# Kernel optimization log

Hardware: AMD Instinct MI355X
Metric: run time of the kernel (lower is better)

The kernel has to match this reference:

```python
import jax, jax.numpy as jnp
import numpy as np

L = 3  # len(context)

def _scale_zp_int8(vmin, vmax):
    # calcScaleZeroPointInt8: qmin=-127, qmax=127
    scale = (vmax - vmin) / 254.0
    initial_zp = -127.0 - vmin / scale
    # clamp to [-127,127] then int() (trunc toward zero)
    zp = jnp.trunc(jnp.clip(initial_zp, -127.0, 127.0)).astype(jnp.int32)
    return scale, zp


def setup_inputs() -> dict:
    key = jax.random.key(0)
    k1, k2, k3 = jax.random.split(key, 3)
    mb, N, D, O = 1, 16386, 1024, 2048
    x = jax.random.normal(k1, (mb, N, D), dtype=jnp.float32)
    W = jax.random.normal(k2, (O, D * L), dtype=jnp.float32) * 0.05
    b = jax.random.normal(k3, (O, 1), dtype=jnp.float32) * 0.1
    return {
        "input": x,
        "weight": W,
        "bias": b,
        "input_min": jnp.min(x),
        "input_max": jnp.max(x),
    }


def reference(input, weight, bias, input_min, input_max):
    mb, N, D = input.shape
    T = N - L + 1  # expected_N
    # im2col-style context gather: window of L consecutive frames -> [mb, T, D*L]
    padded = jnp.concatenate([input[:, i:i + T, :] for i in range(L)], axis=2)

    # weight quantization (int8, symmetric range [-127,127])
    w_scale, w_zp = _scale_zp_int8(jnp.min(weight), jnp.max(weight))
    qw = jnp.round(weight / w_scale + w_zp).astype(jnp.int8)            # [O, K]
    dequant_weight = (qw.astype(jnp.float32) - w_zp.astype(jnp.float32)) * w_scale

    # input quantization
    in_scale, in_zp = _scale_zp_int8(input_min, input_max)
    qx = jnp.round(padded / in_scale + in_zp).astype(jnp.int8)          # [mb, T, K]

    qx32 = qx.astype(jnp.int32)
    qw32 = qw.astype(jnp.int32)

    # int32 GEMM + zero-point correction terms
    x1 = jnp.einsum('btk,ok->bto', qx32, qw32)      # [mb, T, O] int32
    x2 = in_zp * jnp.sum(qw32, axis=1)              # [O]
    x3 = w_zp * jnp.sum(qx32, axis=2)               # [mb, T]

    K = weight.shape[1]
    x = (x1 - x2)[0].T - x3.reshape(-1)             # [O, T]
    x = x + K * w_zp * in_zp
    x = x.T[None].astype(jnp.float32) * (in_scale * w_scale)  # [1, T, O]
    x = x + bias.T                                  # bias [O,1] -> broadcast [1,O]
    return (x, dequant_weight, bias)
```

## Files before the change

kernel.cpp:

```cpp
#include <hip/hip_runtime.h>
#include <stdint.h>

typedef __attribute__((ext_vector_type(4))) int i32x4;

#define N_FRAMES 16386
#define D_DIM    1024
#define O_DIM    2048
#define L_CTX    3
#define K_DIM    3072
#define T_DIM    16384
#define NKT      24

#define WS_PART   0u
#define WS_PARAMS 8192u
#define WS_CO     16384u
#define WS_S      32768u
#define WS_QW     262144u
#define WS_QX     8388608u

struct Params {
  float w_scale, in_scale, cscale;
  int   w_zp, in_zp, konst;
};

typedef __attribute__((address_space(3))) void       lds_void;
typedef const __attribute__((address_space(1))) void gbl_void;

__device__ __forceinline__ unsigned flip_f(float f) {
  unsigned u = __float_as_uint(f);
  return (u & 0x80000000u) ? ~u : (u | 0x80000000u);
}
__device__ __forceinline__ float unflip_f(unsigned v) {
  unsigned u = (v & 0x80000000u) ? (v ^ 0x80000000u) : ~v;
  return __uint_as_float(u);
}

__global__ __launch_bounds__(256) void wminmax_kernel(const float4* __restrict__ w,
                                                      uint2* __restrict__ part, int n4) {
  unsigned lmin = 0xFFFFFFFFu, lmax = 0u;
  for (int i = blockIdx.x * blockDim.x + threadIdx.x; i < n4; i += gridDim.x * blockDim.x) {
    float4 v = w[i];
    unsigned a = flip_f(v.x), b = flip_f(v.y), c = flip_f(v.z), d = flip_f(v.w);
    lmin = min(lmin, min(min(a, b), min(c, d)));
    lmax = max(lmax, max(max(a, b), max(c, d)));
  }
#pragma unroll
  for (int off = 32; off > 0; off >>= 1) {
    lmin = min(lmin, (unsigned)__shfl_xor((int)lmin, off, 64));
    lmax = max(lmax, (unsigned)__shfl_xor((int)lmax, off, 64));
  }
  __shared__ unsigned rmn[4], rmx[4];
  const int wv = threadIdx.x >> 6;
  if ((threadIdx.x & 63) == 0) { rmn[wv] = lmin; rmx[wv] = lmax; }
  __syncthreads();
  if (threadIdx.x == 0) {
    unsigned mn = min(min(rmn[0], rmn[1]), min(rmn[2], rmn[3]));
    unsigned mx = max(max(rmx[0], rmx[1]), max(rmx[2], rmx[3]));
    part[blockIdx.x] = make_uint2(mn, mx);
  }
}

__global__ __launch_bounds__(256) void params_kernel(const uint2* __restrict__ part,
                                                     const float* __restrict__ in_min,
                                                     const float* __restrict__ in_max,
                                                     Params* __restrict__ p) {
  const int t = threadIdx.x;
  uint2 a = part[t], b = part[t + 256];
  unsigned mn = min(a.x, b.x), mx = max(a.y, b.y);
#pragma unroll
  for (int off = 32; off > 0; off >>= 1) {
    mn = min(mn, (unsigned)__shfl_xor((int)mn, off, 64));
    mx = max(mx, (unsigned)__shfl_xor((int)mx, off, 64));
  }
  __shared__ unsigned rmn[4], rmx[4];
  const int wv = t >> 6;
  if ((t & 63) == 0) { rmn[wv] = mn; rmx[wv] = mx; }
  __syncthreads();
  if (t == 0) {
    float wmin = unflip_f(min(min(rmn[0], rmn[1]), min(rmn[2], rmn[3])));
    float wmax = unflip_f(max(max(rmx[0], rmx[1]), max(rmx[2], rmx[3])));
    float ws = (wmax - wmin) / 254.0f;
    float wz = -127.0f - wmin / ws;
    wz = fminf(fmaxf(wz, -127.0f), 127.0f);
    int wzp = (int)wz;
    float imin = *in_min, imax = *in_max;
    float is = (imax - imin) / 254.0f;
    float iz = -127.0f - imin / is;
    iz = fminf(fmaxf(iz, -127.0f), 127.0f);
    int izp = (int)iz;
    p->w_scale = ws; p->in_scale = is; p->cscale = is * ws;
    p->w_zp = wzp;   p->in_zp = izp;
    p->konst = K_DIM * wzp * izp;
  }
}

__global__ __launch_bounds__(256) void quantw_kernel(
    const float* __restrict__ w, const float* __restrict__ bias,
    const Params* __restrict__ p, int8_t* __restrict__ qw,
    int* __restrict__ co, float* __restrict__ dq, float* __restrict__ bias_out) {
  const int o = blockIdx.x;
  const float ws = p->w_scale;
  const float zpf = (float)p->w_zp;
  const float* wrow = w + (size_t)o * K_DIM;
  float* dqrow = dq + (size_t)o * K_DIM;
  int8_t* qrow = qw + (size_t)o * K_DIM;
  int sum = 0;
#pragma unroll
  for (int pass = 0; pass < 3; ++pass) {
    const int k = (pass << 10) + (threadIdx.x << 2);
    float4 v = *(const float4*)(wrow + k);
    int8_t c0 = (int8_t)(int)rintf(v.x / ws + zpf);
    int8_t c1 = (int8_t)(int)rintf(v.y / ws + zpf);
    int8_t c2 = (int8_t)(int)rintf(v.z / ws + zpf);
    int8_t c3 = (int8_t)(int)rintf(v.w / ws + zpf);
    sum += (int)c0 + (int)c1 + (int)c2 + (int)c3;
    unsigned packed = (unsigned)(uint8_t)c0 | ((unsigned)(uint8_t)c1 << 8)
                    | ((unsigned)(uint8_t)c2 << 16) | ((unsigned)(uint8_t)c3 << 24);
    *(unsigned*)(qrow + k) = packed;
    float4 d;
    d.x = ((float)c0 - zpf) * ws;
    d.y = ((float)c1 - zpf) * ws;
    d.z = ((float)c2 - zpf) * ws;
    d.w = ((float)c3 - zpf) * ws;
    *(float4*)(dqrow + k) = d;
  }
  __shared__ int red[4];
#pragma unroll
  for (int off = 32; off > 0; off >>= 1) sum += __shfl_xor(sum, off, 64);
  if ((threadIdx.x & 63) == 0) red[threadIdx.x >> 6] = sum;
  __syncthreads();
  if (threadIdx.x == 0) {
    int tot = red[0] + red[1] + red[2] + red[3];
    co[o] = -p->in_zp * tot;
    bias_out[o] = bias[o];
  }
}

__global__ __launch_bounds__(256) void quantx_kernel(
    const float* __restrict__ x, const Params* __restrict__ p,
    int8_t* __restrict__ qx, int* __restrict__ s) {
  const int n = blockIdx.x;
  const float is = p->in_scale;
  const float zpf = (float)p->in_zp;
  const float4 v = *((const float4*)(x + (size_t)n * D_DIM) + threadIdx.x);
  int8_t c0 = (int8_t)(int)rintf(v.x / is + zpf);
  int8_t c1 = (int8_t)(int)rintf(v.y / is + zpf);
  int8_t c2 = (int8_t)(int)rintf(v.z / is + zpf);
  int8_t c3 = (int8_t)(int)rintf(v.w / is + zpf);
  unsigned packed = (unsigned)(uint8_t)c0 | ((unsigned)(uint8_t)c1 << 8)
                  | ((unsigned)(uint8_t)c2 << 16) | ((unsigned)(uint8_t)c3 << 24);
  ((unsigned*)(qx + (size_t)n * D_DIM))[threadIdx.x] = packed;
  int sum = (int)c0 + (int)c1 + (int)c2 + (int)c3;
  __shared__ int red[4];
#pragma unroll
  for (int off = 32; off > 0; off >>= 1) sum += __shfl_xor(sum, off, 64);
  if ((threadIdx.x & 63) == 0) red[threadIdx.x >> 6] = sum;
  __syncthreads();
  if (threadIdx.x == 0) s[n] = red[0] + red[1] + red[2] + red[3];
}

__global__ __launch_bounds__(512, 2) void gemm_kernel(
    const int8_t* __restrict__ qx, const int8_t* __restrict__ qw,
    const int* __restrict__ co, const int* __restrict__ s,
    const float* __restrict__ bias, const Params* __restrict__ p,
    float* __restrict__ out) {
  __shared__ int8_t A_lds[2][256 * 128];
  __shared__ int8_t B_lds[2][256 * 128];

  const int bid = blockIdx.x;
  const int tn = bid & 7;
  const int tm = bid >> 3;
  const int m0 = tm << 8, n0 = tn << 8;
  const int tid = threadIdx.x;
  const int lane = tid & 63, wave = tid >> 6;
  const int wm = wave >> 2, wn = wave & 3;
  const int lr = lane & 15, kg = lane >> 4;
  const int lr7 = lane & 7;

  const int st_row = tid >> 3;
  const int st_sc  = ((tid & 7) ^ (st_row & 7)) << 4;
  const int8_t* qxa = qx + (size_t)(m0 + st_row) * D_DIM + st_sc;
  const int8_t* qwb = qw + (size_t)(n0 + st_row) * K_DIM + st_sc;

  const int c0 = (kg ^ lr7) << 4;
  const int arow = ((wm << 7) + lr) << 7;
  const int brow = ((wn << 6) + lr) << 7;

  i32x4 a[8][2], b[4][2];
  i32x4 acc[8][4] = {};

  auto stageA = [&](int buf, int kt) {
    const int8_t* sp = qxa + (kt << 7);
#pragma unroll
    for (int j = 0; j < 4; ++j)
      __builtin_amdgcn_global_load_lds((gbl_void*)(sp + (size_t)(j << 6) * D_DIM),
          (lds_void*)(&A_lds[buf][(j << 13) + (wave << 10)]), 16, 0, 0);
  };
  auto stageB = [&](int buf, int kt) {
    const int8_t* sp = qwb + (kt << 7);
#pragma unroll
    for (int j = 0; j < 4; ++j)
      __builtin_amdgcn_global_load_lds((gbl_void*)(sp + (size_t)(j << 6) * K_DIM),
          (lds_void*)(&B_lds[buf][(j << 13) + (wave << 10)]), 16, 0, 0);
  };
  auto read_full = [&](int bf) {
#pragma unroll
    for (int ks = 0; ks < 2; ++ks) {
#pragma unroll
      for (int m = 0; m < 8; ++m)
        a[m][ks] = *(const i32x4*)&A_lds[bf][arow + (m << 11) + (c0 ^ (ks << 6))];
#pragma unroll
      for (int n = 0; n < 4; ++n)
        b[n][ks] = *(const i32x4*)&B_lds[bf][brow + (n << 11) + (c0 ^ (ks << 6))];
    }
  };

  stageA(0, 0); stageB(0, 0);
  stageA(1, 1); stageB(1, 1);
  asm volatile("s_waitcnt vmcnt(8)" ::: "memory");
  __builtin_amdgcn_s_barrier();
  read_full(0);

  for (int kt = 0; kt < NKT; ++kt) {
    const int buf = kt & 1, nxt = buf ^ 1;

    asm volatile("s_waitcnt lgkmcnt(0)" ::: "memory");
    __builtin_amdgcn_s_setprio(1);
#pragma unroll
    for (int m = 0; m < 8; ++m)
#pragma unroll
      for (int n = 0; n < 4; ++n)
#pragma unroll
        for (int ks = 0; ks < 2; ++ks)
          acc[m][n] = __builtin_amdgcn_mfma_i32_16x16x64_i8(a[m][ks], b[n][ks], acc[m][n], 0, 0, 0);
    __builtin_amdgcn_s_setprio(0);

    if (kt + 1 < NKT) {
      asm volatile("s_waitcnt vmcnt(0)" ::: "memory");
      __builtin_amdgcn_s_barrier();
      read_full(nxt);
      if (kt + 2 < NKT) { stageA(buf, kt + 2); stageB(buf, kt + 2); }
    }
  }

  const float cscale = p->cscale;
  const int   wzp    = p->w_zp;
  const int   konst  = p->konst;
  int   cov[4];
  float bov[4];
#pragma unroll
  for (int n = 0; n < 4; ++n) {
    const int o_ = n0 + (wn << 6) + (n << 4) + lr;
    cov[n] = co[o_];
    bov[n] = bias[o_];
  }
#pragma unroll
  for (int m = 0; m < 8; ++m) {
    const int tbase = m0 + (wm << 7) + (m << 4) + (kg << 2);
    int sv[6];
#pragma unroll
    for (int r = 0; r < 6; ++r) sv[r] = s[tbase + r];
    int ctv[4];
#pragma unroll
    for (int r = 0; r < 4; ++r) ctv[r] = konst - wzp * (sv[r] + sv[r + 1] + sv[r + 2]);
#pragma unroll
    for (int n = 0; n < 4; ++n) {
      const int o_ = n0 + (wn << 6) + (n << 4) + lr;
#pragma unroll
      for (int r = 0; r < 4; ++r) {
        out[(size_t)(tbase + r) * O_DIM + o_] =
            (float)(acc[m][n][r] + cov[n] + ctv[r]) * cscale + bov[n];
      }
    }
  }
}

extern "C" void kernel_launch(void* const* d_in, const int* in_sizes, int n_in,
                              void* d_out, int out_size, void* d_ws, size_t ws_size,
                              hipStream_t stream) {
  const float* x      = (const float*)d_in[0];
  const float* w      = (const float*)d_in[1];
  const float* bias   = (const float*)d_in[2];
  const float* in_min = (const float*)d_in[3];
  const float* in_max = (const float*)d_in[4];
  float* out = (float*)d_out;

  uint8_t* ws = (uint8_t*)d_ws;
  uint2*    part = (uint2*)(ws + WS_PART);
  Params*   prm  = (Params*)(ws + WS_PARAMS);
  int*      co   = (int*)(ws + WS_CO);
  int*      s    = (int*)(ws + WS_S);
  int8_t*   qw   = (int8_t*)(ws + WS_QW);
  int8_t*   qx   = (int8_t*)(ws + WS_QX);

  float* dq_out   = out + (size_t)T_DIM * O_DIM;
  float* bias_out = dq_out + (size_t)O_DIM * K_DIM;

  wminmax_kernel<<<512, 256, 0, stream>>>((const float4*)w, part, O_DIM * K_DIM / 4);
  params_kernel<<<1, 256, 0, stream>>>(part, in_min, in_max, prm);
  quantw_kernel<<<O_DIM, 256, 0, stream>>>(w, bias, prm, qw, co, dq_out, bias_out);
  quantx_kernel<<<N_FRAMES, 256, 0, stream>>>(x, prm, qx, s);
  gemm_kernel<<<(T_DIM / 256) * (O_DIM / 256), 512, 0, stream>>>(qx, qw, co, s, bias, prm, out);
}
```

Before: 135.8 us.

## Switch GEMM to 64-wide K tiles with triple-buffered LDS and interleaved reads

Halves the K tile to 64 bytes and replaces the double-buffered LDS pipeline with a three-stage ring. Each stage is issued before the MFMAs, and the next tile's A fragments are read from LDS in between the MFMA groups, so loads overlap compute. The per-stage footprint shrinks and the swizzled layout is dropped for a plain row layout. This risks more LDS bank conflicts, and there are twice as many barriers per K pass.

```diff
diff --git a/kernel.cpp b/kernel.cpp
--- a/kernel.cpp
+++ b/kernel.cpp
@@ -9,7 +9,7 @@
 #define L_CTX    3
 #define K_DIM    3072
 #define T_DIM    16384
-#define NKT      24
+#define NKT      48
 
 #define WS_PART   0u
 #define WS_PARAMS 8192u
@@ -159,13 +159,36 @@
   if (threadIdx.x == 0) s[n] = red[0] + red[1] + red[2] + red[3];
 }
 
+#define ITERX(KT, RB, SB)                                                      \
+  {                                                                            \
+    asm volatile("s_waitcnt lgkmcnt(0)" ::: "memory");                         \
+    if ((KT) + 2 < NKT) stage(SB, (KT) + 2);                                   \
+    __builtin_amdgcn_s_setprio(1);                                             \
+    _Pragma("unroll")                                                          \
+    for (int m = 0; m < 8; ++m) {                                              \
+      _Pragma("unroll")                                                        \
+      for (int n = 0; n < 4; ++n)                                              \
+        acc[m][n] = __builtin_amdgcn_mfma_i32_16x16x64_i8(a[m], b[n], acc[m][n], 0, 0, 0); \
+      if ((KT) + 1 < NKT)                                                      \
+        a[m] = *(const i32x4*)&A_lds[RB][arow + (m << 10) + kgo];              \
+    }                                                                          \
+    __builtin_amdgcn_s_setprio(0);                                             \
+    if ((KT) + 1 < NKT) {                                                      \
+      _Pragma("unroll")                                                        \
+      for (int n = 0; n < 4; ++n)                                              \
+        b[n] = *(const i32x4*)&B_lds[RB][brow + (n << 10) + kgo];              \
+      asm volatile("s_waitcnt vmcnt(0)" ::: "memory");                         \
+      __builtin_amdgcn_s_barrier();                                            \
+    }                                                                          \
+  }
+
 __global__ __launch_bounds__(512, 2) void gemm_kernel(
     const int8_t* __restrict__ qx, const int8_t* __restrict__ qw,
     const int* __restrict__ co, const int* __restrict__ s,
     const float* __restrict__ bias, const Params* __restrict__ p,
     float* __restrict__ out) {
-  __shared__ int8_t A_lds[2][256 * 128];
-  __shared__ int8_t B_lds[2][256 * 128];
+  __shared__ int8_t A_lds[3][16384];
+  __shared__ int8_t B_lds[3][16384];
 
   const int bid = blockIdx.x;
   const int tn = bid & 7;
@@ -175,72 +198,45 @@
   const int lane = tid & 63, wave = tid >> 6;
   const int wm = wave >> 2, wn = wave & 3;
   const int lr = lane & 15, kg = lane >> 4;
-  const int lr7 = lane & 7;
-
-  const int st_row = tid >> 3;
-  const int st_sc  = ((tid & 7) ^ (st_row & 7)) << 4;
-  const int8_t* qxa = qx + (size_t)(m0 + st_row) * D_DIM + st_sc;
-  const int8_t* qwb = qw + (size_t)(n0 + st_row) * K_DIM + st_sc;
-
-  const int c0 = (kg ^ lr7) << 4;
-  const int arow = ((wm << 7) + lr) << 7;
-  const int brow = ((wn << 6) + lr) << 7;
-
-  i32x4 a[8][2], b[4][2];
+  const int kgo = kg << 4;
+
+  const int8_t* qxa = qx + (size_t)(m0 + (lane >> 2)) * D_DIM + ((lane & 3) << 4);
+  const int8_t* qwb = qw + (size_t)(n0 + (lane >> 2)) * K_DIM + ((lane & 3) << 4);
+
+  const int arow = ((wm << 7) + lr) << 6;
+  const int brow = ((wn << 6) + lr) << 6;
+
+  i32x4 a[8], b[4];
   i32x4 acc[8][4] = {};
 
-  auto stageA = [&](int buf, int kt) {
-    const int8_t* sp = qxa + (kt << 7);
-#pragma unroll
-    for (int j = 0; j < 4; ++j)
-      __builtin_amdgcn_global_load_lds((gbl_void*)(sp + (size_t)(j << 6) * D_DIM),
-          (lds_void*)(&A_lds[buf][(j << 13) + (wave << 10)]), 16, 0, 0);
-  };
-  auto stageB = [&](int buf, int kt) {
-    const int8_t* sp = qwb + (kt << 7);
-#pragma unroll
-    for (int j = 0; j < 4; ++j)
-      __builtin_amdgcn_global_load_lds((gbl_void*)(sp + (size_t)(j << 6) * K_DIM),
-          (lds_void*)(&B_lds[buf][(j << 13) + (wave << 10)]), 16, 0, 0);
-  };
-  auto read_full = [&](int bf) {
-#pragma unroll
-    for (int ks = 0; ks < 2; ++ks) {
-#pragma unroll
-      for (int m = 0; m < 8; ++m)
-        a[m][ks] = *(const i32x4*)&A_lds[bf][arow + (m << 11) + (c0 ^ (ks << 6))];
-#pragma unroll
-      for (int n = 0; n < 4; ++n)
-        b[n][ks] = *(const i32x4*)&B_lds[bf][brow + (n << 11) + (c0 ^ (ks << 6))];
+  auto stage = [&](int sb, int kt) {
+#pragma unroll
+    for (int e = 0; e < 2; ++e) {
+      const int ev = (wave << 1) + e;
+      __builtin_amdgcn_global_load_lds(
+          (gbl_void*)(qxa + (size_t)(ev << 4) * D_DIM + (kt << 6)),
+          (lds_void*)(&A_lds[sb][ev << 10]), 16, 0, 0);
+      __builtin_amdgcn_global_load_lds(
+          (gbl_void*)(qwb + (size_t)(ev << 4) * K_DIM + (kt << 6)),
+          (lds_void*)(&B_lds[sb][ev << 10]), 16, 0, 0);
     }
   };
 
-  stageA(0, 0); stageB(0, 0);
-  stageA(1, 1); stageB(1, 1);
-  asm volatile("s_waitcnt vmcnt(8)" ::: "memory");
+  stage(0, 0);
+  stage(1, 1);
+  asm volatile("s_waitcnt vmcnt(0)" ::: "memory");
   __builtin_amdgcn_s_barrier();
-  read_full(0);
-
-  for (int kt = 0; kt < NKT; ++kt) {
-    const int buf = kt & 1, nxt = buf ^ 1;
-
-    asm volatile("s_waitcnt lgkmcnt(0)" ::: "memory");
-    __builtin_amdgcn_s_setprio(1);
-#pragma unroll
-    for (int m = 0; m < 8; ++m)
-#pragma unroll
-      for (int n = 0; n < 4; ++n)
-#pragma unroll
-        for (int ks = 0; ks < 2; ++ks)
-          acc[m][n] = __builtin_amdgcn_mfma_i32_16x16x64_i8(a[m][ks], b[n][ks], acc[m][n], 0, 0, 0);
-    __builtin_amdgcn_s_setprio(0);
-
-    if (kt + 1 < NKT) {
-      asm volatile("s_waitcnt vmcnt(0)" ::: "memory");
-      __builtin_amdgcn_s_barrier();
-      read_full(nxt);
-      if (kt + 2 < NKT) { stageA(buf, kt + 2); stageB(buf, kt + 2); }
-    }
+#pragma unroll
+  for (int m = 0; m < 8; ++m)
+    a[m] = *(const i32x4*)&A_lds[0][arow + (m << 10) + kgo];
+#pragma unroll
+  for (int n = 0; n < 4; ++n)
+    b[n] = *(const i32x4*)&B_lds[0][brow + (n << 10) + kgo];
+
+  for (int kt = 0; kt < NKT; kt += 3) {
+    ITERX(kt + 0, 1, 2);
+    ITERX(kt + 1, 2, 0);
+    ITERX(kt + 2, 0, 1);
   }
 
   const float cscale = p->cscale;
```

Measured after the change: 153.7 us. 1.13x slower.
